# Kernel optimization log

Hardware: AMD Instinct MI355X
Metric: run time of the kernel (lower is better)

Reference implementation:

```python
import jax, jax.numpy as jnp
import numpy as np

B, N, E = 256, 256, 512
ITER = 10

def setup_inputs() -> dict:
    key = jax.random.key(0)
    k1, k2, k3 = jax.random.split(key, 3)
    feats = jax.random.normal(k1, (B, N, E), dtype=jnp.float32)
    logits = jax.random.normal(k2, (B, N, 1), dtype=jnp.float32)
    # nn.Parameter initialized to zeros in the original; use small random values
    # so the CRF update is non-trivial for correctness checking.
    W = jax.random.normal(k3, (1, N, N), dtype=jnp.float32) * 0.01
    return {"feats": feats, "logits": logits, "W": W}

def reference(feats, logits, W):
    # cosine similarity between all node pairs: [B, N, N]
    feats_norm = jnp.linalg.norm(feats, axis=2, keepdims=True)          # [B,N,1]
    pairwise_norm = feats_norm @ jnp.swapaxes(feats_norm, 1, 2)         # [B,N,N]
    pairwise_dot = jnp.einsum('bne,bme->bnm', feats, feats)             # [B,N,N]
    pairwise_sim = pairwise_dot / pairwise_norm
    W_sym = (W + jnp.swapaxes(W, 1, 2)) * 0.5                           # [1,N,N]
    pairwise_potential = pairwise_sim * W_sym                           # [B,N,N]
    unary_potential = logits                                            # [B,N,1]

    def step(lg, _):
        probs = jnp.swapaxes(jax.nn.sigmoid(lg), 1, 2)                  # [B,1,N]
        # probs*P - (1-probs)*P == (2*probs - 1)*P
        e = jnp.sum((2.0 * probs - 1.0) * pairwise_potential,
                    axis=2, keepdims=True)                              # [B,N,1]
        return unary_potential + e, None

    out, _ = jax.lax.scan(step, logits, None, length=ITER)
    return out
```

## Files before the change

kernel.cpp:

```cpp
#include <hip/hip_runtime.h>
#include <hip/hip_bf16.h>
#include <math.h>

#define Bb   256
#define Nn   256
#define Ee   512
#define TKF  64
#define NCH  (Ee / TKF)
#define NITER 10

typedef __attribute__((ext_vector_type(8))) short bf16x8;
typedef __attribute__((ext_vector_type(4))) float f32x4;

typedef __attribute__((address_space(1))) const void glb_cv;
typedef __attribute__((address_space(3))) void lds_v;

static __device__ __forceinline__ unsigned short f2bf(float f) {
    __hip_bfloat16 h = __float2bfloat16(f);
    return __builtin_bit_cast(unsigned short, h);
}

static __device__ __forceinline__ bf16x8 ldfrag(const float* tb, int row, int kb) {
    const int sw = (row & 7) << 4;
    const char* base = reinterpret_cast<const char*>(tb) + row * 256;
    const float4 a = *reinterpret_cast<const float4*>(base + (((kb * 4) + 0) ^ sw));
    const float4 b = *reinterpret_cast<const float4*>(base + (((kb * 4) + 16) ^ sw));
    bf16x8 r;
    r[0] = f2bf(a.x); r[1] = f2bf(a.y); r[2] = f2bf(a.z); r[3] = f2bf(a.w);
    r[4] = f2bf(b.x); r[5] = f2bf(b.y); r[6] = f2bf(b.z); r[7] = f2bf(b.w);
    return r;
}

__global__ __launch_bounds__(512, 2) void crf_mfma(
    const float* __restrict__ feats,
    const float* __restrict__ logits,
    const float* __restrict__ W,
    float* __restrict__ out)
{
    const int b    = blockIdx.x;
    const int t    = threadIdx.x;
    const int wave = t >> 6;
    const int lane = t & 63;
    const int wr   = wave >> 1;
    const int wc   = wave & 1;
    const int lo   = lane & 15;
    const int hi   = lane >> 4;

    __shared__ float tile[2 * Nn * TKF];
    __shared__ float invn[Nn];
    __shared__ float svec[Nn];
    __shared__ float uvec[Nn];
    __shared__ float lgv[Nn];
    __shared__ float part[4][Nn];

    f32x4 acc[4][8];
#pragma unroll
    for (int i = 0; i < 4; ++i)
#pragma unroll
        for (int j = 0; j < 8; ++j) acc[i][j] = (f32x4){0.f, 0.f, 0.f, 0.f};

    const float* Fb = feats + (size_t)b * Nn * Ee;

    auto stage = [&](int ch, int buf) {
        float* tbase = tile + buf * (Nn * TKF);
#pragma unroll
        for (int i = 0; i < 8; ++i) {
            const int r0s = wave * 32 + i * 4;
            const int row = r0s + (lane >> 4);
            const int g16 = (lane & 15) ^ (row & 7);
            const float* src = Fb + (size_t)row * Ee + ch * TKF + g16 * 4;
            __builtin_amdgcn_global_load_lds((glb_cv*)src,
                                             (lds_v*)(tbase + r0s * TKF), 16, 0, 0);
        }
    };

    stage(0, 0);
    if (t < Nn) {
        const float u = logits[(size_t)b * Nn + t];
        uvec[t] = u;
        lgv[t]  = u;
    }
    __syncthreads();

    for (int ch = 0; ch < NCH; ++ch) {
        const int buf = ch & 1;
        if (ch + 1 < NCH) stage(ch + 1, buf ^ 1);
        const float* tb = tile + buf * (Nn * TKF);
#pragma unroll
        for (int ks = 0; ks < 2; ++ks) {
            const int kb = ks * 32 + hi * 8;
            bf16x8 af[4];
#pragma unroll
            for (int rb = 0; rb < 4; ++rb)
                af[rb] = ldfrag(tb, wr * 64 + rb * 16 + lo, kb);
#pragma unroll
            for (int cg = 0; cg < 2; ++cg) {
                bf16x8 bfv[4];
#pragma unroll
                for (int cq = 0; cq < 4; ++cq)
                    bfv[cq] = ldfrag(tb, wc * 128 + (cg * 4 + cq) * 16 + lo, kb);
#pragma unroll
                for (int rb = 0; rb < 4; ++rb)
#pragma unroll
                    for (int cq = 0; cq < 4; ++cq)
                        acc[rb][cg * 4 + cq] = __builtin_amdgcn_mfma_f32_16x16x32_bf16(
                            af[rb], bfv[cq], acc[rb][cg * 4 + cq], 0, 0, 0);
            }
        }
        __syncthreads();
    }

#pragma unroll
    for (int rb = 0; rb < 4; ++rb) {
        const int rowbase = wr * 64 + rb * 16;
#pragma unroll
        for (int cb = 0; cb < 8; ++cb) {
            const int colbase = wc * 128 + cb * 16;
            if (rowbase == colbase) {
#pragma unroll
                for (int r = 0; r < 4; ++r) {
                    if (hi * 4 + r == lo)
                        invn[rowbase + hi * 4 + r] = 1.0f / sqrtf(acc[rb][cb][r]);
                }
            }
        }
    }
    __syncthreads();

#pragma unroll
    for (int rb = 0; rb < 4; ++rb) {
        const int rbase = wr * 64 + rb * 16 + hi * 4;
        const float4 ir4 = *reinterpret_cast<const float4*>(&invn[rbase]);
        const float ir[4] = {ir4.x, ir4.y, ir4.z, ir4.w};
#pragma unroll
        for (int cb = 0; cb < 8; ++cb) {
            const int col = wc * 128 + cb * 16 + lo;
            const float ic = invn[col];
            const float4 wt = *reinterpret_cast<const float4*>(&W[col * Nn + rbase]);
            const float wtr[4] = {wt.x, wt.y, wt.z, wt.w};
#pragma unroll
            for (int r = 0; r < 4; ++r) {
                const float wsym = 0.5f * (W[(rbase + r) * Nn + col] + wtr[r]);
                acc[rb][cb][r] = acc[rb][cb][r] * ir[r] * ic * wsym;
            }
        }
    }

    for (int itr = 0; itr < NITER; ++itr) {
        if (t < Nn) {
            const float x = lgv[t];
            svec[t] = 2.f / (1.f + __expf(-x)) - 1.f;
        }
        __syncthreads();

        float ep[8] = {0.f, 0.f, 0.f, 0.f, 0.f, 0.f, 0.f, 0.f};
#pragma unroll
        for (int rb = 0; rb < 4; ++rb) {
            const float4 s4 = *reinterpret_cast<const float4*>(
                &svec[wr * 64 + rb * 16 + hi * 4]);
#pragma unroll
            for (int cb = 0; cb < 8; ++cb)
                ep[cb] += acc[rb][cb][0] * s4.x + acc[rb][cb][1] * s4.y
                        + acc[rb][cb][2] * s4.z + acc[rb][cb][3] * s4.w;
        }
#pragma unroll
        for (int cb = 0; cb < 8; ++cb) {
            ep[cb] += __shfl_xor(ep[cb], 16);
            ep[cb] += __shfl_xor(ep[cb], 32);
        }
        if (lane < 16) {
#pragma unroll
            for (int cb = 0; cb < 8; ++cb)
                part[wr][wc * 128 + cb * 16 + lane] = ep[cb];
        }
        __syncthreads();
        if (t < Nn)
            lgv[t] = uvec[t] + part[0][t] + part[1][t] + part[2][t] + part[3][t];
    }

    if (t < Nn) out[(size_t)b * Nn + t] = lgv[t];
}

extern "C" void kernel_launch(void* const* d_in, const int* in_sizes, int n_in,
                              void* d_out, int out_size, void* d_ws, size_t ws_size,
                              hipStream_t stream) {
    const float* feats  = (const float*)d_in[0];
    const float* logits = (const float*)d_in[1];
    const float* W      = (const float*)d_in[2];
    float* out = (float*)d_out;

    crf_mfma<<<dim3(Bb), dim3(512), 0, stream>>>(feats, logits, W, out);
}
```

Before: 55.47 us.

## Convert staged fp32 tiles to bf16 LDS once and precompute symmetric W

Each staged fp32 chunk is now converted once into a swizzled bf16 LDS tile, so the MFMA fragment loads read bf16 directly instead of every wave converting floats on each load. This replaces the double-buffered fp32 tile with a single fp32 staging buffer plus a bf16 tile. It also adds a sync per chunk and serialises the convert step against staging the next chunk. Separately, a small pre-kernel writes the symmetric W to workspace when one is available, avoiding transposed strided reads of W in every block.

```diff
diff --git a/kernel.cpp b/kernel.cpp
--- a/kernel.cpp
+++ b/kernel.cpp
@@ -20,21 +20,31 @@
     return __builtin_bit_cast(unsigned short, h);
 }
 
-static __device__ __forceinline__ bf16x8 ldfrag(const float* tb, int row, int kb) {
-    const int sw = (row & 7) << 4;
-    const char* base = reinterpret_cast<const char*>(tb) + row * 256;
-    const float4 a = *reinterpret_cast<const float4*>(base + (((kb * 4) + 0) ^ sw));
-    const float4 b = *reinterpret_cast<const float4*>(base + (((kb * 4) + 16) ^ sw));
-    bf16x8 r;
-    r[0] = f2bf(a.x); r[1] = f2bf(a.y); r[2] = f2bf(a.z); r[3] = f2bf(a.w);
-    r[4] = f2bf(b.x); r[5] = f2bf(b.y); r[6] = f2bf(b.z); r[7] = f2bf(b.w);
-    return r;
-}
-
+static __device__ __forceinline__ bf16x8 ldfrag(const unsigned char* bt, int row, int ks, int hi) {
+    const int byte = row * 128 + (((ks * 64 + hi * 16)) ^ ((row & 7) << 4));
+    return *reinterpret_cast<const bf16x8*>(bt + byte);
+}
+
+__global__ __launch_bounds__(256) void wsym_k(const float* __restrict__ W,
+                                              float* __restrict__ wsym) {
+    const int idx = blockIdx.x * 256 + threadIdx.x;
+    const int r  = idx >> 6;
+    const int c0 = (idx & 63) * 4;
+    const float4 a = *reinterpret_cast<const float4*>(&W[r * Nn + c0]);
+    float4 o;
+    o.x = 0.5f * (a.x + W[(c0 + 0) * Nn + r]);
+    o.y = 0.5f * (a.y + W[(c0 + 1) * Nn + r]);
+    o.z = 0.5f * (a.z + W[(c0 + 2) * Nn + r]);
+    o.w = 0.5f * (a.w + W[(c0 + 3) * Nn + r]);
+    *reinterpret_cast<float4*>(&wsym[r * Nn + c0]) = o;
+}
+
+template <bool USE_WS>
 __global__ __launch_bounds__(512, 2) void crf_mfma(
     const float* __restrict__ feats,
     const float* __restrict__ logits,
     const float* __restrict__ W,
+    const float* __restrict__ wsym,
     float* __restrict__ out)
 {
     const int b    = blockIdx.x;
@@ -46,7 +56,8 @@
     const int lo   = lane & 15;
     const int hi   = lane >> 4;
 
-    __shared__ float tile[2 * Nn * TKF];
+    __shared__ float fstage[Nn * TKF];
+    __shared__ unsigned char btile[Nn * 128];
     __shared__ float invn[Nn];
     __shared__ float svec[Nn];
     __shared__ float uvec[Nn];
@@ -61,20 +72,32 @@
 
     const float* Fb = feats + (size_t)b * Nn * Ee;
 
-    auto stage = [&](int ch, int buf) {
-        float* tbase = tile + buf * (Nn * TKF);
+    auto stage = [&](int ch) {
 #pragma unroll
         for (int i = 0; i < 8; ++i) {
             const int r0s = wave * 32 + i * 4;
             const int row = r0s + (lane >> 4);
-            const int g16 = (lane & 15) ^ (row & 7);
-            const float* src = Fb + (size_t)row * Ee + ch * TKF + g16 * 4;
+            const float* src = Fb + (size_t)row * Ee + ch * TKF + (lane & 15) * 4;
             __builtin_amdgcn_global_load_lds((glb_cv*)src,
-                                             (lds_v*)(tbase + r0s * TKF), 16, 0, 0);
+                                             (lds_v*)(fstage + r0s * TKF), 16, 0, 0);
         }
     };
 
-    stage(0, 0);
+    auto convert = [&]() {
+#pragma unroll
+        for (int g = 0; g < 8; ++g) {
+            const int m   = t + 512 * g;
+            const int row = m >> 4;
+            const int gc  = m & 15;
+            const float4 v = *reinterpret_cast<const float4*>(fstage + m * 4);
+            ushort4 pk;
+            pk.x = f2bf(v.x); pk.y = f2bf(v.y); pk.z = f2bf(v.z); pk.w = f2bf(v.w);
+            *reinterpret_cast<ushort4*>(
+                btile + row * 128 + ((gc * 8) ^ ((row & 7) << 4))) = pk;
+        }
+    };
+
+    stage(0);
     if (t < Nn) {
         const float u = logits[(size_t)b * Nn + t];
         uvec[t] = u;
@@ -83,22 +106,21 @@
     __syncthreads();
 
     for (int ch = 0; ch < NCH; ++ch) {
-        const int buf = ch & 1;
-        if (ch + 1 < NCH) stage(ch + 1, buf ^ 1);
-        const float* tb = tile + buf * (Nn * TKF);
+        convert();
+        __syncthreads();
+        if (ch + 1 < NCH) stage(ch + 1);
 #pragma unroll
         for (int ks = 0; ks < 2; ++ks) {
-            const int kb = ks * 32 + hi * 8;
             bf16x8 af[4];
 #pragma unroll
             for (int rb = 0; rb < 4; ++rb)
-                af[rb] = ldfrag(tb, wr * 64 + rb * 16 + lo, kb);
+                af[rb] = ldfrag(btile, wr * 64 + rb * 16 + lo, ks, hi);
 #pragma unroll
             for (int cg = 0; cg < 2; ++cg) {
                 bf16x8 bfv[4];
 #pragma unroll
                 for (int cq = 0; cq < 4; ++cq)
-                    bfv[cq] = ldfrag(tb, wc * 128 + (cg * 4 + cq) * 16 + lo, kb);
+                    bfv[cq] = ldfrag(btile, wc * 128 + (cg * 4 + cq) * 16 + lo, ks, hi);
 #pragma unroll
                 for (int rb = 0; rb < 4; ++rb)
 #pragma unroll
@@ -136,12 +158,20 @@
         for (int cb = 0; cb < 8; ++cb) {
             const int col = wc * 128 + cb * 16 + lo;
             const float ic = invn[col];
-            const float4 wt = *reinterpret_cast<const float4*>(&W[col * Nn + rbase]);
-            const float wtr[4] = {wt.x, wt.y, wt.z, wt.w};
-#pragma unroll
-            for (int r = 0; r < 4; ++r) {
-                const float wsym = 0.5f * (W[(rbase + r) * Nn + col] + wtr[r]);
-                acc[rb][cb][r] = acc[rb][cb][r] * ir[r] * ic * wsym;
+            if (USE_WS) {
+#pragma unroll
+                for (int r = 0; r < 4; ++r) {
+                    const float ws = wsym[(rbase + r) * Nn + col];
+                    acc[rb][cb][r] = acc[rb][cb][r] * ir[r] * ic * ws;
+                }
+            } else {
+                const float4 wt = *reinterpret_cast<const float4*>(&W[col * Nn + rbase]);
+                const float wtr[4] = {wt.x, wt.y, wt.z, wt.w};
+#pragma unroll
+                for (int r = 0; r < 4; ++r) {
+                    const float ws = 0.5f * (W[(rbase + r) * Nn + col] + wtr[r]);
+                    acc[rb][cb][r] = acc[rb][cb][r] * ir[r] * ic * ws;
+                }
             }
         }
     }
@@ -189,5 +219,11 @@
     const float* W      = (const float*)d_in[2];
     float* out = (float*)d_out;
 
-    crf_mfma<<<dim3(Bb), dim3(512), 0, stream>>>(feats, logits, W, out);
-}
+    if (ws_size >= (size_t)Nn * Nn * sizeof(float)) {
+        float* wsym = (float*)d_ws;
+        wsym_k<<<dim3(64), dim3(256), 0, stream>>>(W, wsym);
+        crf_mfma<true><<<dim3(Bb), dim3(512), 0, stream>>>(feats, logits, W, wsym, out);
+    } else {
+        crf_mfma<false><<<dim3(Bb), dim3(512), 0, stream>>>(feats, logits, W, nullptr, out);
+    }
+}
```

After: 48.67 us. 12.3% less time.
